# Kernel optimization log

Measured on AMD Instinct MI355X. Metric: run time of the kernel, lower is better.

The kernel has to match this reference:

```python
import jax, jax.numpy as jnp
import numpy as np

SEQ = 4096
BLOCK = 64            # sparse_block_size
BLOCKS = SEQ // BLOCK # 64 block rows/cols
NUM_ORACLES = 32
ORACLE = SEQ // NUM_ORACLES      # 128
LOCAL_BLOCKS = ORACLE // BLOCK   # 2 (sliding-window width in blocks)
PATTERN_ID = 0


def _build_block_mask(pattern_id=PATTERN_ID):
    # Mirrors DKernelPredefinedSparseAttention.__init__ create_mask((i,))
    q_pos = np.arange(BLOCKS)[:, None]
    k_pos = np.arange(BLOCKS)[None, :]
    causal = q_pos >= k_pos
    sliding = (q_pos - k_pos) < LOCAL_BLOCKS
    vert = np.zeros(BLOCKS, dtype=bool)
    real_col = int(pattern_id * ORACLE + 0.5)
    cs = real_col // BLOCK
    ce = (real_col + ORACLE) // BLOCK
    vert[cs:ce] = True
    vert[0:1] = True  # global block 0 always visible
    return causal & (sliding | vert[None, :])


def setup_inputs() -> dict:
    key = jax.random.key(0)
    kq, kk, kv = jax.random.split(key, 3)
    shape = (1, SEQ, 8, 128)  # bshd, matches module's own smoke test layout
    q = jax.random.normal(kq, shape, dtype=jnp.float32)
    k = jax.random.normal(kk, shape, dtype=jnp.float32)
    v = jax.random.normal(kv, shape, dtype=jnp.float32)
    block_mask = jnp.asarray(_build_block_mask())  # [BLOCKS, BLOCKS] bool
    return {"q": q, "k": k, "v": v, "block_mask": block_mask}


def reference(q, k, v, block_mask):
    # Expand block-level mask to token level: [S, S]
    tok_mask = jnp.repeat(jnp.repeat(block_mask, BLOCK, axis=0), BLOCK, axis=1)
    scale = 1.0 / jnp.sqrt(jnp.asarray(q.shape[-1], q.dtype))
    # bshd x bshd -> bhqk scores
    scores = jnp.einsum("bqhd,bkhd->bhqk", q, k) * scale
    neg = jnp.asarray(-1e30, scores.dtype)
    scores = jnp.where(tok_mask[None, None, :, :], scores, neg)
    probs = jax.nn.softmax(scores, axis=-1)
    out = jnp.einsum("bhqk,bkhd->bqhd", probs, v)
    return out
```

## Files before the change

kernel.cpp:

```cpp
#include <hip/hip_runtime.h>
#include <hip/hip_bf16.h>

typedef __bf16 bf16x8 __attribute__((ext_vector_type(8)));
typedef float floatx4 __attribute__((ext_vector_type(4)));

constexpr int SEQ = 4096;
constexpr int NH  = 8;
constexpr int DH  = 128;
constexpr int BLK = 64;
constexpr int QBLOCKS = SEQ / BLK;
constexpr int ROWSTRIDE = NH * DH;
constexpr float SCALE = 0.088388347648318447f;

__device__ __forceinline__ bool buf_is_bf16(const unsigned* w) {
    int cnt = 0;
#pragma unroll 1
    for (int i = 0; i < 128; ++i) {
        unsigned e = (w[i] >> 7) & 0xFFu;
        cnt += (e >= 96u && e <= 134u) ? 1 : 0;
    }
    return cnt >= 96;
}

template<bool IS_BF16> struct IO;
template<> struct IO<true> {
    using T = __bf16;
    static __device__ __forceinline__ bf16x8 load8(const T* p) {
        return *(const bf16x8*)p;
    }
};
template<> struct IO<false> {
    using T = float;
    static __device__ __forceinline__ bf16x8 load8(const T* p) {
        float4 a = *(const float4*)p;
        float4 b = *(const float4*)(p + 4);
        bf16x8 r = { (__bf16)a.x, (__bf16)a.y, (__bf16)a.z, (__bf16)a.w,
                     (__bf16)b.x, (__bf16)b.y, (__bf16)b.z, (__bf16)b.w };
        return r;
    }
};

template<bool IS_BF16>
__global__ __launch_bounds__(256) void sparse_attn_kernel(
    const void* __restrict__ Qv,
    const void* __restrict__ Kv,
    const void* __restrict__ Vv,
    void* __restrict__ Outv)
{
    if (buf_is_bf16((const unsigned*)Qv) != IS_BF16) return;

    using T = typename IO<IS_BF16>::T;
    const T* Q = (const T*)Qv;
    const T* K = (const T*)Kv;
    const T* V = (const T*)Vv;
    T* Out = (T*)Outv;

    const int qb   = blockIdx.x;
    const int h    = blockIdx.y;
    const int wave = threadIdx.x >> 6;
    const int lane = threadIdx.x & 63;
    const int quad = lane >> 4;
    const int l16  = lane & 15;

    __shared__ __align__(16) __bf16 p_lds[4][16][BLK + 8];

    const int qrow = qb * BLK + wave * 16 + l16;
    const T* qptr = Q + (size_t)qrow * ROWSTRIDE + h * DH;
    bf16x8 qfrag[4];
#pragma unroll
    for (int s = 0; s < 4; ++s)
        qfrag[s] = IO<IS_BF16>::load8(qptr + s * 32 + quad * 8);

    floatx4 o_acc[8];
#pragma unroll
    for (int n = 0; n < 8; ++n) o_acc[n] = floatx4{0.f, 0.f, 0.f, 0.f};
    float m_run[4], l_run[4];
#pragma unroll
    for (int r = 0; r < 4; ++r) { m_run[r] = -1e30f; l_run[r] = 0.f; }

    int blist[4];
    int nb = 0;
    {
        int cand[4] = {0, 1, qb - 1, qb};
        for (int i = 0; i < 4; ++i) {
            int b = cand[i];
            if (b < 0 || b > qb) continue;
            bool dup = false;
            for (int j = 0; j < nb; ++j) dup = dup || (blist[j] == b);
            if (!dup) blist[nb++] = b;
        }
    }

    for (int bi = 0; bi < nb; ++bi) {
        const int kb = blist[bi];

        floatx4 sfrag[4];
#pragma unroll
        for (int n = 0; n < 4; ++n) {
            floatx4 c = floatx4{0.f, 0.f, 0.f, 0.f};
            const T* kptr =
                K + (size_t)(kb * BLK + n * 16 + l16) * ROWSTRIDE + h * DH;
#pragma unroll
            for (int s = 0; s < 4; ++s) {
                bf16x8 kf = IO<IS_BF16>::load8(kptr + s * 32 + quad * 8);
                c = __builtin_amdgcn_mfma_f32_16x16x32_bf16(qfrag[s], kf, c, 0, 0, 0);
            }
            sfrag[n] = c;
        }

        float mnew[4];
#pragma unroll
        for (int r = 0; r < 4; ++r) {
            float mx = m_run[r];
#pragma unroll
            for (int n = 0; n < 4; ++n) {
                sfrag[n][r] *= SCALE;
                mx = fmaxf(mx, sfrag[n][r]);
            }
#pragma unroll
            for (int off = 1; off < 16; off <<= 1)
                mx = fmaxf(mx, __shfl_xor(mx, off, 64));
            mnew[r] = mx;
        }
#pragma unroll
        for (int r = 0; r < 4; ++r) {
            float alpha = __expf(m_run[r] - mnew[r]);
            float rs = 0.f;
#pragma unroll
            for (int n = 0; n < 4; ++n) {
                float p = __expf(sfrag[n][r] - mnew[r]);
                sfrag[n][r] = p;
                rs += p;
            }
#pragma unroll
            for (int off = 1; off < 16; off <<= 1)
                rs += __shfl_xor(rs, off, 64);
            l_run[r] = l_run[r] * alpha + rs;
            m_run[r] = mnew[r];
#pragma unroll
            for (int n = 0; n < 8; ++n) o_acc[n][r] *= alpha;
        }

#pragma unroll
        for (int n = 0; n < 4; ++n)
#pragma unroll
            for (int r = 0; r < 4; ++r)
                p_lds[wave][quad * 4 + r][n * 16 + l16] = (__bf16)sfrag[n][r];
        __syncthreads();

#pragma unroll
        for (int s2 = 0; s2 < 2; ++s2) {
            bf16x8 pa = *(const bf16x8*)&p_lds[wave][l16][s2 * 32 + quad * 8];
            const T* vptr =
                V + (size_t)(kb * BLK + s2 * 32 + quad * 8) * ROWSTRIDE + h * DH + l16;
#pragma unroll
            for (int n = 0; n < 8; ++n) {
                bf16x8 vb;
#pragma unroll
                for (int j = 0; j < 8; ++j)
                    vb[j] = (__bf16)vptr[(size_t)j * ROWSTRIDE + n * 16];
                o_acc[n] = __builtin_amdgcn_mfma_f32_16x16x32_bf16(pa, vb, o_acc[n], 0, 0, 0);
            }
        }
        __syncthreads();
    }

    const int orow_base = qb * BLK + wave * 16 + quad * 4;
#pragma unroll
    for (int r = 0; r < 4; ++r) {
        float inv = 1.f / l_run[r];
        T* optr = Out + (size_t)(orow_base + r) * ROWSTRIDE + h * DH + l16;
#pragma unroll
        for (int n = 0; n < 8; ++n)
            optr[n * 16] = (T)(o_acc[n][r] * inv);
    }
}

extern "C" void kernel_launch(void* const* d_in, const int* in_sizes, int n_in,
                              void* d_out, int out_size, void* d_ws, size_t ws_size,
                              hipStream_t stream) {
    const void* Q = d_in[0];
    const void* K = d_in[1];
    const void* V = d_in[2];

    dim3 grid(QBLOCKS, NH);
    dim3 block(256);
    sparse_attn_kernel<true ><<<grid, block, 0, stream>>>(Q, K, V, d_out);
    sparse_attn_kernel<false><<<grid, block, 0, stream>>>(Q, K, V, d_out);
}
```

Measured before the change: 138.0 us.

## Stage V tiles cooperatively in double-buffered LDS and drop bf16 dtype-probe launch

Removes the runtime dtype detection and the second templated kernel launch, specialising for fp32 inputs only. V blocks are now loaded cooperatively by all 256 threads, converted to bf16 and stored in a double-buffered LDS layout that matches the MFMA B-operand. The next block is prefetched while the current one is computed, replacing redundant strided per-wave global gathers. Barrier placement changes to one sync per iteration, which relies on the double buffer and per-wave P tiles for correctness.

```diff
diff --git a/kernel.cpp b/kernel.cpp
--- a/kernel.cpp
+++ b/kernel.cpp
@@ -9,67 +9,60 @@
 constexpr int DH  = 128;
 constexpr int BLK = 64;
 constexpr int QBLOCKS = SEQ / BLK;
-constexpr int ROWSTRIDE = NH * DH;
+constexpr int RS = NH * DH;
 constexpr float SCALE = 0.088388347648318447f;
 
-__device__ __forceinline__ bool buf_is_bf16(const unsigned* w) {
-    int cnt = 0;
-#pragma unroll 1
-    for (int i = 0; i < 128; ++i) {
-        unsigned e = (w[i] >> 7) & 0xFFu;
-        cnt += (e >= 96u && e <= 134u) ? 1 : 0;
-    }
-    return cnt >= 96;
+__device__ __forceinline__ bf16x8 load8f(const float* p) {
+    float4 a = *(const float4*)p;
+    float4 b = *(const float4*)(p + 4);
+    bf16x8 r = { (__bf16)a.x, (__bf16)a.y, (__bf16)a.z, (__bf16)a.w,
+                 (__bf16)b.x, (__bf16)b.y, (__bf16)b.z, (__bf16)b.w };
+    return r;
 }
 
-template<bool IS_BF16> struct IO;
-template<> struct IO<true> {
-    using T = __bf16;
-    static __device__ __forceinline__ bf16x8 load8(const T* p) {
-        return *(const bf16x8*)p;
+__device__ __forceinline__ void stage_v(const float* __restrict__ V,
+                                        int kb, int h, int n_t, int kh,
+                                        __bf16* __restrict__ dst) {
+    const float* base = V + (size_t)(kb * BLK + kh * 32) * RS + h * DH + n_t;
+    const int nt = n_t >> 4;
+    const int lbase = n_t & 15;
+#pragma unroll
+    for (int g = 0; g < 4; ++g) {
+        bf16x8 pk;
+#pragma unroll
+        for (int j = 0; j < 8; ++j)
+            pk[j] = (__bf16)base[(size_t)(g * 8 + j) * RS];
+        __bf16* d = dst + ((size_t)((kh * 8 + nt) * 64 + lbase + 16 * g)) * 8;
+        *(bf16x8*)d = pk;
     }
-};
-template<> struct IO<false> {
-    using T = float;
-    static __device__ __forceinline__ bf16x8 load8(const T* p) {
-        float4 a = *(const float4*)p;
-        float4 b = *(const float4*)(p + 4);
-        bf16x8 r = { (__bf16)a.x, (__bf16)a.y, (__bf16)a.z, (__bf16)a.w,
-                     (__bf16)b.x, (__bf16)b.y, (__bf16)b.z, (__bf16)b.w };
-        return r;
-    }
-};
+}
 
-template<bool IS_BF16>
 __global__ __launch_bounds__(256) void sparse_attn_kernel(
-    const void* __restrict__ Qv,
-    const void* __restrict__ Kv,
-    const void* __restrict__ Vv,
-    void* __restrict__ Outv)
+    const float* __restrict__ Q,
+    const float* __restrict__ K,
+    const float* __restrict__ V,
+    float* __restrict__ Out)
 {
-    if (buf_is_bf16((const unsigned*)Qv) != IS_BF16) return;
-
-    using T = typename IO<IS_BF16>::T;
-    const T* Q = (const T*)Qv;
-    const T* K = (const T*)Kv;
-    const T* V = (const T*)Vv;
-    T* Out = (T*)Outv;
-
     const int qb   = blockIdx.x;
     const int h    = blockIdx.y;
-    const int wave = threadIdx.x >> 6;
-    const int lane = threadIdx.x & 63;
+    const int tid  = threadIdx.x;
+    const int wave = tid >> 6;
+    const int lane = tid & 63;
     const int quad = lane >> 4;
     const int l16  = lane & 15;
 
+    __shared__ __align__(16) __bf16 v_lds[2][2][8][64][8];
     __shared__ __align__(16) __bf16 p_lds[4][16][BLK + 8];
 
+    const int n_t = tid & 127;
+    const int kh  = tid >> 7;
+
     const int qrow = qb * BLK + wave * 16 + l16;
-    const T* qptr = Q + (size_t)qrow * ROWSTRIDE + h * DH;
+    const float* qp = Q + (size_t)qrow * RS + h * DH;
     bf16x8 qfrag[4];
 #pragma unroll
     for (int s = 0; s < 4; ++s)
-        qfrag[s] = IO<IS_BF16>::load8(qptr + s * 32 + quad * 8);
+        qfrag[s] = load8f(qp + s * 32 + quad * 8);
 
     floatx4 o_acc[8];
 #pragma unroll
@@ -91,18 +84,26 @@
         }
     }
 
+    stage_v(V, blist[0], h, n_t, kh, &v_lds[0][0][0][0][0]);
+
     for (int bi = 0; bi < nb; ++bi) {
-        const int kb = blist[bi];
+        __syncthreads();
+        if (bi + 1 < nb)
+            stage_v(V, blist[bi + 1], h, n_t, kh,
+                    &v_lds[(bi + 1) & 1][0][0][0][0]);
+
+        const int kb  = blist[bi];
+        const int buf = bi & 1;
 
         floatx4 sfrag[4];
 #pragma unroll
         for (int n = 0; n < 4; ++n) {
             floatx4 c = floatx4{0.f, 0.f, 0.f, 0.f};
-            const T* kptr =
-                K + (size_t)(kb * BLK + n * 16 + l16) * ROWSTRIDE + h * DH;
+            const float* kp =
+                K + (size_t)(kb * BLK + n * 16 + l16) * RS + h * DH;
 #pragma unroll
             for (int s = 0; s < 4; ++s) {
-                bf16x8 kf = IO<IS_BF16>::load8(kptr + s * 32 + quad * 8);
+                bf16x8 kf = load8f(kp + s * 32 + quad * 8);
                 c = __builtin_amdgcn_mfma_f32_16x16x32_bf16(qfrag[s], kf, c, 0, 0, 0);
             }
             sfrag[n] = c;
@@ -146,45 +147,38 @@
 #pragma unroll
             for (int r = 0; r < 4; ++r)
                 p_lds[wave][quad * 4 + r][n * 16 + l16] = (__bf16)sfrag[n][r];
-        __syncthreads();
 
 #pragma unroll
         for (int s2 = 0; s2 < 2; ++s2) {
             bf16x8 pa = *(const bf16x8*)&p_lds[wave][l16][s2 * 32 + quad * 8];
-            const T* vptr =
-                V + (size_t)(kb * BLK + s2 * 32 + quad * 8) * ROWSTRIDE + h * DH + l16;
 #pragma unroll
             for (int n = 0; n < 8; ++n) {
-                bf16x8 vb;
-#pragma unroll
-                for (int j = 0; j < 8; ++j)
-                    vb[j] = (__bf16)vptr[(size_t)j * ROWSTRIDE + n * 16];
+                bf16x8 vb = *(const bf16x8*)&v_lds[buf][s2][n][lane][0];
                 o_acc[n] = __builtin_amdgcn_mfma_f32_16x16x32_bf16(pa, vb, o_acc[n], 0, 0, 0);
             }
         }
-        __syncthreads();
     }
 
     const int orow_base = qb * BLK + wave * 16 + quad * 4;
 #pragma unroll
     for (int r = 0; r < 4; ++r) {
         float inv = 1.f / l_run[r];
-        T* optr = Out + (size_t)(orow_base + r) * ROWSTRIDE + h * DH + l16;
+        float* op = Out + (size_t)(orow_base + r) * RS + h * DH + l16;
 #pragma unroll
         for (int n = 0; n < 8; ++n)
-            optr[n * 16] = (T)(o_acc[n][r] * inv);
+            op[n * 16] = o_acc[n][r] * inv;
     }
 }
 
 extern "C" void kernel_launch(void* const* d_in, const int* in_sizes, int n_in,
                               void* d_out, int out_size, void* d_ws, size_t ws_size,
                               hipStream_t stream) {
-    const void* Q = d_in[0];
-    const void* K = d_in[1];
-    const void* V = d_in[2];
+    const float* Q = (const float*)d_in[0];
+    const float* K = (const float*)d_in[1];
+    const float* V = (const float*)d_in[2];
+    float* Out = (float*)d_out;
 
     dim3 grid(QBLOCKS, NH);
     dim3 block(256);
-    sparse_attn_kernel<true ><<<grid, block, 0, stream>>>(Q, K, V, d_out);
-    sparse_attn_kernel<false><<<grid, block, 0, stream>>>(Q, K, V, d_out);
+    sparse_attn_kernel<<<grid, block, 0, stream>>>(Q, K, V, Out);
 }
```

Result: faster. 125.9 us (-8.7%).
